# Kernel optimization log

Measured on AMD Instinct MI355X. Metric: run time of the kernel, lower is better.

## Reference

```python
import jax, jax.numpy as jnp
import numpy as np

NEG = -1e10  # the original uses -10000000000.0
B, T, L = 64, 512, 64
START, END = 0, L - 1


def setup_inputs() -> dict:
    key = jax.random.key(0)
    k_em, k_tr, k_len = jax.random.split(key, 3)
    emission_scores = jax.random.normal(k_em, (B, T, L), dtype=jnp.float32)
    # transition initialized as in __init__: randn with start column / end row masked
    transition = jax.random.normal(k_tr, (L, L), dtype=jnp.float32)
    transition = transition.at[:, START].set(NEG)
    transition = transition.at[END, :].set(NEG)
    sent_lens = jax.random.randint(k_len, (B,), T // 2, T + 1, dtype=jnp.int32)
    return {"emission_scores": emission_scores, "transition": transition,
            "sent_lens": sent_lens}


def reference(emission_scores, transition, sent_lens):
    # --- calculate_all_scores ---
    em = emission_scores.at[:, :, START].set(NEG).at[:, :, END].set(NEG)
    # scores[b,t,y_prev,y_t] = transition[y_prev,y_t] + emission[b,t,y_t]
    scores = transition[None, None, :, :] + em[:, :, None, :]  # [B,T,L,L]
    scores = scores.at[:, 1:, START, :].set(NEG)

    # --- forward_score: sequential DP via scan ---
    alpha0 = scores[:, 0, START, :]  # [B,L]

    def step(alpha_prev, s_t):  # s_t: [B,L,L]
        alpha_t = jax.nn.logsumexp(alpha_prev[:, :, None] + s_t, axis=1)
        return alpha_t, alpha_t

    _, alphas_rest = jax.lax.scan(step, alpha0, jnp.moveaxis(scores[:, 1:], 1, 0))
    alpha = jnp.concatenate([alpha0[:, None, :], jnp.moveaxis(alphas_rest, 0, 1)],
                            axis=1)  # [B,T,L]

    idx = (sent_lens - 1).astype(jnp.int32)[:, None, None]  # [B,1,1]
    last_alpha = jnp.take_along_axis(alpha, idx, axis=1)[:, 0, :]  # [B,L]
    last_alpha = last_alpha + transition[:, END][None, :]
    log_Z = jax.nn.logsumexp(last_alpha, axis=1)  # [B]
    return alpha, log_Z
```

## Files before the change

### kernel.cpp

```cpp
#include <hip/hip_runtime.h>

#define NEGV -10000000000.0f
constexpr int Bn = 64, Tn = 512, Ln = 64;
constexpr int CK = 32;
constexpr int NC = 16;
constexpr int QP = 68;

typedef float f32x16 __attribute__((ext_vector_type(16)));
typedef __bf16 bf16x8 __attribute__((ext_vector_type(8)));
typedef unsigned int u32;
typedef unsigned short u16;

__device__ inline float waveMaxF(float v) {
#pragma unroll
    for (int off = 32; off > 0; off >>= 1)
        v = fmaxf(v, __shfl_xor(v, off, 64));
    return v;
}
__device__ inline u32 packbf(float a, float b) {
    u32 ua = __float_as_uint(a) + 0x8000u;
    u32 ub = __float_as_uint(b) + 0x8000u;
    return (ua >> 16) | (ub & 0xffff0000u);
}
__device__ inline float lo16f(u32 d) { return __uint_as_float(d << 16); }
__device__ inline float hi16f(u32 d) { return __uint_as_float(d & 0xffff0000u); }

template <bool FIRST>
__device__ void chunk_scan(const float* __restrict__ emb,
                           float* __restrict__ outb, float* uLDS,
                           const float* Ecol, float entry, int t0, int j, int len,
                           float trSj, float* aLastOut, float* aFinalOut) {
    const bool edge = (j == 0) || (j == Ln - 1);
    float emq[4];
#pragma unroll
    for (int tt = 0; tt < 4; ++tt) {
        float v = emb[(t0 + tt) * Ln + j];
        emq[tt] = edge ? NEGV : v;
    }
    float aPrev, mPrev, u;
    int tauStart;
    if (FIRST) {
        float a0 = trSj + emq[0];
        outb[t0 * Ln + j] = a0;
        aPrev = a0;
        mPrev = __shfl(a0, 1, 64);
        u = __expf(a0 - mPrev);
        tauStart = 1;
    } else {
        aPrev = entry;
        mPrev = __shfl(entry, 1, 64);
        u = __expf(entry - mPrev);
        tauStart = 0;
    }
    float aLast = *aLastOut;
#pragma unroll 4
    for (int tau = tauStart; tau < CK; ++tau) {
        const int t = t0 + tau;
        uLDS[j] = u;
        const float em_t = emq[tau & 3];
        const int tp = tau + 4;
        if (tp < CK) {
            float v = emb[(t0 + tp) * Ln + j];
            emq[tp & 3] = edge ? NEGV : v;
        }
        float mNext = __shfl(aPrev, 1, 64);
        float cf = __expf(em_t + (mPrev - mNext));
        float acc0 = 0.f, acc1 = 0.f, acc2 = 0.f, acc3 = 0.f;
        const float4* u4 = reinterpret_cast<const float4*>(uLDS);
#pragma unroll
        for (int i4 = 0; i4 < 16; ++i4) {
            float4 uv = u4[i4];
            acc0 = fmaf(uv.x, Ecol[4 * i4 + 0], acc0);
            acc1 = fmaf(uv.y, Ecol[4 * i4 + 1], acc1);
            acc2 = fmaf(uv.z, Ecol[4 * i4 + 2], acc2);
            acc3 = fmaf(uv.w, Ecol[4 * i4 + 3], acc3);
        }
        float S = (acc0 + acc1) + (acc2 + acc3);
        float lg = __logf(S);
        lg = (S > 0.f) ? lg : NEGV;
        float a_t = em_t + (mPrev + lg);
        outb[t * Ln + j] = a_t;
        if (t == len - 1) aLast = a_t;
        u = S * cf;
        aPrev = a_t;
        mPrev = mNext;
    }
    *aLastOut = aLast;
    *aFinalOut = aPrev;
}

__global__ __launch_bounds__(128) void crf_passA(const float* __restrict__ em,
                                                 const float* __restrict__ tr,
                                                 float* __restrict__ out,
                                                 float* __restrict__ wsE,
                                                 float* __restrict__ wsS) {
    const int b = blockIdx.x & 63;
    const int cix = blockIdx.x >> 6;
    const int J = threadIdx.x >> 6;
    const int L = threadIdx.x & 63;
    __shared__ alignas(16) float gtab[CK * 64];
    __shared__ alignas(16) u16 Qlds[64 * QP];
    __shared__ alignas(16) float uLDS[64];
    __shared__ float sLDS[2];
    __shared__ float sigLDS[2];

    if (cix == 0) {
        if (J == 1) return;
        float Ecol[Ln];
#pragma unroll
        for (int i = 0; i < Ln; ++i) Ecol[i] = __expf(tr[i * Ln + L]);
        const float trSj = tr[L];
        const float* emb = em + (size_t)b * Tn * Ln;
        float* outb = out + (size_t)b * Tn * Ln;
        float dummyLast = 0.f, aFinal;
        chunk_scan<true>(emb, outb, uLDS, Ecol, 0.f, 0, L,  -1, trSj, &dummyLast, &aFinal);
        wsE[b * 1024 + 1 * 64 + L] = aFinal;
        return;
    }

    const int t0 = CK * cix;
    const int c31 = L & 31;
    const int h = L >> 5;

    {
        float orig[16], sv[16];
        const int tb = t0 + 16 * J;
#pragma unroll
        for (int r = 0; r < 16; ++r) {
            float v = em[((size_t)b * Tn + (tb + r)) * Ln + L];
            if (L == 0 || L == Ln - 1) v = NEGV;
            orig[r] = v;
            sv[r] = v;
        }
#pragma unroll
        for (int off = 32; off > 0; off >>= 1) {
#pragma unroll
            for (int r = 0; r < 16; ++r)
                sv[r] = fmaxf(sv[r], __shfl_xor(sv[r], off, 64));
        }
        float ssum = 0.f;
#pragma unroll
        for (int r = 0; r < 16; ++r) {
            gtab[(16 * J + r) * 64 + L] = __expf(orig[r] - sv[r]);
            ssum += sv[r];
        }
        if (L == 0) sLDS[J] = ssum;
    }
    __syncthreads();
    const float sSum = sLDS[0] + sLDS[1];

    uint4 Ap[2][4];
#pragma unroll
    for (int I = 0; I < 2; ++I)
#pragma unroll
        for (int kc = 0; kc < 4; ++kc) {
            float e[8];
#pragma unroll
            for (int q = 0; q < 8; ++q) {
                int k = 16 * kc + 8 * h + q;
                e[q] = __expf(tr[k * Ln + 32 * I + c31]);
            }
            Ap[I][kc] = make_uint4(packbf(e[0], e[1]), packbf(e[2], e[3]),
                                   packbf(e[4], e[5]), packbf(e[6], e[7]));
        }

    const int n = 32 * J + c31;
    {
        const float* trn = tr + n * Ln + 32 * h;
        const float* g0 = gtab + 32 * h;
#pragma unroll
        for (int k4 = 0; k4 < 8; ++k4) {
            float v0 = __expf(trn[4 * k4 + 0]) * g0[4 * k4 + 0];
            float v1 = __expf(trn[4 * k4 + 1]) * g0[4 * k4 + 1];
            float v2 = __expf(trn[4 * k4 + 2]) * g0[4 * k4 + 2];
            float v3 = __expf(trn[4 * k4 + 3]) * g0[4 * k4 + 3];
            uint2 w;
            w.x = packbf(v0, v1);
            w.y = packbf(v2, v3);
            *(uint2*)&Qlds[n * QP + 32 * h + 4 * k4] = w;
        }
    }

    float sig_w = 0.f;
    float wm = 1.0f;
    const f32x16 Z = (f32x16)(0.0f);
    for (int tau = 1; tau < CK; ++tau) {
        uint4 Bp[4];
#pragma unroll
        for (int kc = 0; kc < 4; ++kc) {
            const u16* p = &Qlds[n * QP + 16 * kc + 8 * h];
            uint2 q0 = *(const uint2*)(p);
            uint2 q1 = *(const uint2*)(p + 4);
            Bp[kc] = make_uint4(q0.x, q0.y, q1.x, q1.y);
        }
        f32x16 acc0 = Z, acc1 = Z;
#pragma unroll
        for (int kc = 0; kc < 4; ++kc) {
            acc0 = __builtin_amdgcn_mfma_f32_32x32x16_bf16(
                __builtin_bit_cast(bf16x8, Ap[0][kc]),
                __builtin_bit_cast(bf16x8, Bp[kc]), acc0, 0, 0, 0);
            acc1 = __builtin_amdgcn_mfma_f32_32x32x16_bf16(
                __builtin_bit_cast(bf16x8, Ap[1][kc]),
                __builtin_bit_cast(bf16x8, Bp[kc]), acc1, 0, 0, 0);
        }
        const bool doRescale = ((tau & 3) == 0);
        const bool doMeasure = ((tau & 3) == 2);
        float rr = 1.0f;
        if (doRescale) {
            rr = 1.0f / wm;
            sig_w += __logf(wm);
        }
        float lmax = 0.f;
#pragma unroll
        for (int I = 0; I < 2; ++I) {
#pragma unroll
            for (int rg = 0; rg < 4; ++rg) {
                const int k0 = 32 * I + 8 * rg + 4 * h;
                float4 G = *(const float4*)&gtab[tau * 64 + k0];
                float v0 = (I ? acc1 : acc0)[4 * rg + 0] * (G.x * rr);
                float v1 = (I ? acc1 : acc0)[4 * rg + 1] * (G.y * rr);
                float v2 = (I ? acc1 : acc0)[4 * rg + 2] * (G.z * rr);
                float v3 = (I ? acc1 : acc0)[4 * rg + 3] * (G.w * rr);
                if (doMeasure) lmax = fmaxf(lmax, fmaxf(fmaxf(v0, v1), fmaxf(v2, v3)));
                uint2 w;
                w.x = packbf(v0, v1);
                w.y = packbf(v2, v3);
                *(uint2*)&Qlds[n * QP + k0] = w;
            }
        }
        if (doMeasure) wm = waveMaxF(lmax);
    }

    if (L == 0) sigLDS[J] = sSum + sig_w;
    __syncthreads();
    const float sg0 = sigLDS[0], sg1 = sigLDS[1];
    const float smax = fmaxf(sg0, sg1);
    const float fh = __expf((h ? sg1 : sg0) - smax);
    const int r = 32 * J + c31;
    float rv[32];
    float lmaxr = 0.f;
#pragma unroll
    for (int i = 0; i < 32; ++i) {
        float v = __uint_as_float(((u32)Qlds[(32 * h + i) * QP + r]) << 16) * fh;
        rv[i] = v;
        lmaxr = fmaxf(lmaxr, v);
    }
    float rmax = fmaxf(lmaxr, __shfl_xor(lmaxr, 32, 64));
    float inv = (rmax > 0.f) ? 1.0f / rmax : 0.f;
    float sj = (rmax > 0.f) ? smax + __logf(rmax) : 0.f;
    u32* og = (u32*)out + (size_t)b * (Tn * Ln) + (size_t)cix * (CK * Ln) + r * 32 + h * 16;
#pragma unroll
    for (int w8 = 0; w8 < 4; ++w8) {
        uint4 w;
        w.x = packbf(rv[8 * w8 + 0] * inv, rv[8 * w8 + 1] * inv);
        w.y = packbf(rv[8 * w8 + 2] * inv, rv[8 * w8 + 3] * inv);
        w.z = packbf(rv[8 * w8 + 4] * inv, rv[8 * w8 + 5] * inv);
        w.w = packbf(rv[8 * w8 + 6] * inv, rv[8 * w8 + 7] * inv);
        *(uint4*)(og + 4 * w8) = w;
    }
    if (h == 0) wsS[b * 1024 + cix * 64 + r] = sj;
}

__global__ __launch_bounds__(64) void crf_passB(const float* __restrict__ out,
                                                float* __restrict__ wsE,
                                                const float* __restrict__ wsS) {
    const int b = blockIdx.x;
    const int j = threadIdx.x;
    __shared__ alignas(16) float uL[64];
    const u32* Qbase = (const u32*)out + (size_t)b * (Tn * Ln);

    float e = wsE[b * 1024 + 1 * 64 + j];
    uint4 nxt[8];
    float signxt = wsS[b * 1024 + 1 * 64 + j];
#pragma unroll
    for (int r = 0; r < 8; ++r) nxt[r] = *(const uint4*)(Qbase + 1 * (CK * Ln) + j * 32 + 4 * r);

#pragma unroll
    for (int c = 1; c <= 14; ++c) {
        uint4 cur[8];
#pragma unroll
        for (int r = 0; r < 8; ++r) cur[r] = nxt[r];
        float sig = signxt;
        if (c < 14) {
#pragma unroll
            for (int r = 0; r < 8; ++r)
                nxt[r] = *(const uint4*)(Qbase + (size_t)(c + 1) * (CK * Ln) + j * 32 + 4 * r);
            signxt = wsS[b * 1024 + (c + 1) * 64 + j];
        }
        float m = __shfl(e, 1, 64);
        uL[j] = __expf(e - m);
        const float4* u4 = reinterpret_cast<const float4*>(uL);
        float S = 0.f;
#pragma unroll
        for (int i4 = 0; i4 < 16; ++i4) {
            float4 uv = u4[i4];
            u32 d0 = ((const u32*)cur)[2 * i4];
            u32 d1 = ((const u32*)cur)[2 * i4 + 1];
            S = fmaf(uv.x, lo16f(d0), S);
            S = fmaf(uv.y, hi16f(d0), S);
            S = fmaf(uv.z, lo16f(d1), S);
            S = fmaf(uv.w, hi16f(d1), S);
        }
        float a;
        if (S > 0.f) a = m + sig + __logf(S);
        else a = m + NEGV + ((j == 0) ? NEGV : 0.f);
        e = a;
        wsE[b * 1024 + (c + 1) * 64 + j] = e;
    }
}

__global__ __launch_bounds__(64) void crf_passC(const float* __restrict__ em,
                                                const float* __restrict__ tr,
                                                const int* __restrict__ lens,
                                                float* __restrict__ out,
                                                const float* __restrict__ wsE) {
    const int b = blockIdx.x & 63;
    const int cix = 1 + (blockIdx.x >> 6);
    const int j = threadIdx.x;
    __shared__ alignas(16) float uLDS[64];

    float Ecol[Ln];
#pragma unroll
    for (int i = 0; i < Ln; ++i) Ecol[i] = __expf(tr[i * Ln + j]);
    const float trEj = tr[j * Ln + (Ln - 1)];
    const int len = lens[b];
    const float* emb = em + (size_t)b * Tn * Ln;
    float* outb = out + (size_t)b * Tn * Ln;
    const float entry = wsE[b * 1024 + cix * 64 + j];

    float aLast = 0.f, aFinal;
    chunk_scan<false>(emb, outb, uLDS, Ecol, entry, CK * cix, j, len, 0.f, &aLast, &aFinal);

    if (((len - 1) >> 5) == cix) {
        float last = aLast + trEj;
        float m2 = last;
#pragma unroll
        for (int off = 32; off > 0; off >>= 1)
            m2 = fmaxf(m2, __shfl_xor(m2, off, 64));
        float e2 = __expf(last - m2);
#pragma unroll
        for (int off = 32; off > 0; off >>= 1)
            e2 += __shfl_xor(e2, off, 64);
        if (j == 0) out[(size_t)Bn * Tn * Ln + b] = m2 + __logf(e2);
    }
}

__global__ __launch_bounds__(64) void crf_fallback(const float* __restrict__ em,
                                                   const float* __restrict__ tr,
                                                   const int* __restrict__ lens,
                                                   float* __restrict__ out) {
    const int b = blockIdx.x;
    const int j = threadIdx.x;
    __shared__ alignas(16) float uLDS[Ln];
    float E[Ln];
#pragma unroll
    for (int i = 0; i < Ln; ++i) E[i] = __expf(tr[i * Ln + j]);
    const float trSj = tr[j];
    const float trEj = tr[j * Ln + (Ln - 1)];
    const int len = lens[b];
    const bool edge = (j == 0) || (j == Ln - 1);
    const float* emb = em + (size_t)b * Tn * Ln;
    float* outb = out + (size_t)b * Tn * Ln;
    float emq[4];
#pragma unroll
    for (int tt = 0; tt < 4; ++tt) {
        float v = emb[tt * Ln + j];
        emq[tt] = edge ? NEGV : v;
    }
    float a = trSj + emq[0];
    outb[j] = a;
    float aPrev = a, aLast = a;
    float mPrev = __shfl(a, 1, 64);
    float u = __expf(a - mPrev);
#pragma unroll 4
    for (int t = 1; t < Tn; ++t) {
        uLDS[j] = u;
        const float em_t = emq[t & 3];
        const int tp = t + 4;
        if (tp < Tn) {
            float v = emb[tp * Ln + j];
            emq[tp & 3] = edge ? NEGV : v;
        }
        float mNext = __shfl(aPrev, 1, 64);
        float cf = __expf(em_t + (mPrev - mNext));
        float acc0 = 0.f, acc1 = 0.f, acc2 = 0.f, acc3 = 0.f;
        const float4* u4 = reinterpret_cast<const float4*>(uLDS);
#pragma unroll
        for (int i4 = 0; i4 < 16; ++i4) {
            float4 uv = u4[i4];
            acc0 = fmaf(uv.x, E[4 * i4 + 0], acc0);
            acc1 = fmaf(uv.y, E[4 * i4 + 1], acc1);
            acc2 = fmaf(uv.z, E[4 * i4 + 2], acc2);
            acc3 = fmaf(uv.w, E[4 * i4 + 3], acc3);
        }
        float S = (acc0 + acc1) + (acc2 + acc3);
        float lg = __logf(S);
        lg = (S > 0.f) ? lg : NEGV;
        float a_t = em_t + (mPrev + lg);
        outb[t * Ln + j] = a_t;
        if (t == len - 1) aLast = a_t;
        u = S * cf;
        aPrev = a_t;
        mPrev = mNext;
    }
    float last = aLast + trEj;
    float m2 = last;
#pragma unroll
    for (int off = 32; off > 0; off >>= 1)
        m2 = fmaxf(m2, __shfl_xor(m2, off, 64));
    float e2 = __expf(last - m2);
#pragma unroll
    for (int off = 32; off > 0; off >>= 1)
        e2 += __shfl_xor(e2, off, 64);
    if (j == 0) out[(size_t)Bn * Tn * Ln + b] = m2 + __logf(e2);
}

extern "C" void kernel_launch(void* const* d_in, const int* in_sizes, int n_in,
                              void* d_out, int out_size, void* d_ws, size_t ws_size,
                              hipStream_t stream) {
    const float* em = (const float*)d_in[0];
    const float* tr = (const float*)d_in[1];
    const int* lens = (const int*)d_in[2];
    float* out = (float*)d_out;
    const size_t wsNeed = 2u * 64 * 16 * 64 * sizeof(float);
    if (ws_size >= wsNeed) {
        float* wsE = (float*)d_ws;
        float* wsS = wsE + 64 * 16 * 64;
        crf_passA<<<dim3(1024), dim3(128), 0, stream>>>(em, tr, out, wsE, wsS);
        crf_passB<<<dim3(64), dim3(64), 0, stream>>>(out, wsE, wsS);
        crf_passC<<<dim3(960), dim3(64), 0, stream>>>(em, tr, lens, out, wsE);
    } else {
        crf_fallback<<<dim3(Bn), dim3(64), 0, stream>>>(em, tr, lens, out);
    }
}
```

Before: 136.5 us.

## Keep MFMA B operand in registers via permlane32 swap instead of LDS round-trip

The per-step write of the bf16 state to LDS followed by reading it back as the next MFMA B operand is replaced. The accumulator output is packed with the hardware v_cvt_pk_bf16_f32 instruction and rearranged across lane halves with permlane32_swap, so it lands directly in the B-operand layout. LDS is written only once after the loop, and the padding QP drops to 64 since the per-step access pattern no longer needs conflict avoidance. Rounding now uses the hardware conversion instead of the manual add-and-shift, and correctness depends on the swap producing exactly the operand layout.

```diff
diff --git a/kernel.cpp b/kernel.cpp
--- a/kernel.cpp
+++ b/kernel.cpp
@@ -4,12 +4,13 @@
 constexpr int Bn = 64, Tn = 512, Ln = 64;
 constexpr int CK = 32;
 constexpr int NC = 16;
-constexpr int QP = 68;
+constexpr int QP = 64;
 
 typedef float f32x16 __attribute__((ext_vector_type(16)));
 typedef __bf16 bf16x8 __attribute__((ext_vector_type(8)));
 typedef unsigned int u32;
 typedef unsigned short u16;
+typedef unsigned int u32x2 __attribute__((ext_vector_type(2)));
 
 __device__ inline float waveMaxF(float v) {
 #pragma unroll
@@ -21,6 +22,16 @@
     u32 ua = __float_as_uint(a) + 0x8000u;
     u32 ub = __float_as_uint(b) + 0x8000u;
     return (ua >> 16) | (ub & 0xffff0000u);
+}
+__device__ inline u32 cvtpk(float a, float b) {
+    u32 r;
+    asm("v_cvt_pk_bf16_f32 %0, %1, %2" : "=v"(r) : "v"(a), "v"(b));
+    return r;
+}
+__device__ inline void swap32(u32& x, u32& y) {
+    u32x2 r = __builtin_amdgcn_permlane32_swap(x, y, false, false);
+    x = r.x;
+    y = r.y;
 }
 __device__ inline float lo16f(u32 d) { return __uint_as_float(d << 16); }
 __device__ inline float hi16f(u32 d) { return __uint_as_float(d & 0xffff0000u); }
@@ -165,19 +176,19 @@
         }
 
     const int n = 32 * J + c31;
+    uint4 Bp[4];
     {
-        const float* trn = tr + n * Ln + 32 * h;
-        const float* g0 = gtab + 32 * h;
-#pragma unroll
-        for (int k4 = 0; k4 < 8; ++k4) {
-            float v0 = __expf(trn[4 * k4 + 0]) * g0[4 * k4 + 0];
-            float v1 = __expf(trn[4 * k4 + 1]) * g0[4 * k4 + 1];
-            float v2 = __expf(trn[4 * k4 + 2]) * g0[4 * k4 + 2];
-            float v3 = __expf(trn[4 * k4 + 3]) * g0[4 * k4 + 3];
-            uint2 w;
-            w.x = packbf(v0, v1);
-            w.y = packbf(v2, v3);
-            *(uint2*)&Qlds[n * QP + 32 * h + 4 * k4] = w;
+        const float* trn = tr + n * Ln;
+#pragma unroll
+        for (int kc = 0; kc < 4; ++kc) {
+            float v[8];
+#pragma unroll
+            for (int q = 0; q < 8; ++q) {
+                const int k = 16 * kc + 8 * h + q;
+                v[q] = __expf(trn[k]) * gtab[k];
+            }
+            Bp[kc] = make_uint4(cvtpk(v[0], v[1]), cvtpk(v[2], v[3]),
+                                cvtpk(v[4], v[5]), cvtpk(v[6], v[7]));
         }
     }
 
@@ -185,14 +196,6 @@
     float wm = 1.0f;
     const f32x16 Z = (f32x16)(0.0f);
     for (int tau = 1; tau < CK; ++tau) {
-        uint4 Bp[4];
-#pragma unroll
-        for (int kc = 0; kc < 4; ++kc) {
-            const u16* p = &Qlds[n * QP + 16 * kc + 8 * h];
-            uint2 q0 = *(const uint2*)(p);
-            uint2 q1 = *(const uint2*)(p + 4);
-            Bp[kc] = make_uint4(q0.x, q0.y, q1.x, q1.y);
-        }
         f32x16 acc0 = Z, acc1 = Z;
 #pragma unroll
         for (int kc = 0; kc < 4; ++kc) {
@@ -211,25 +214,35 @@
             sig_w += __logf(wm);
         }
         float lmax = 0.f;
+        const float* gt = gtab + tau * 64;
 #pragma unroll
         for (int I = 0; I < 2; ++I) {
+            u32 pp[8];
 #pragma unroll
             for (int rg = 0; rg < 4; ++rg) {
                 const int k0 = 32 * I + 8 * rg + 4 * h;
-                float4 G = *(const float4*)&gtab[tau * 64 + k0];
+                float4 G = *(const float4*)&gt[k0];
                 float v0 = (I ? acc1 : acc0)[4 * rg + 0] * (G.x * rr);
                 float v1 = (I ? acc1 : acc0)[4 * rg + 1] * (G.y * rr);
                 float v2 = (I ? acc1 : acc0)[4 * rg + 2] * (G.z * rr);
                 float v3 = (I ? acc1 : acc0)[4 * rg + 3] * (G.w * rr);
                 if (doMeasure) lmax = fmaxf(lmax, fmaxf(fmaxf(v0, v1), fmaxf(v2, v3)));
-                uint2 w;
-                w.x = packbf(v0, v1);
-                w.y = packbf(v2, v3);
-                *(uint2*)&Qlds[n * QP + k0] = w;
+                pp[2 * rg + 0] = cvtpk(v0, v1);
+                pp[2 * rg + 1] = cvtpk(v2, v3);
             }
+            swap32(pp[0], pp[2]);
+            swap32(pp[1], pp[3]);
+            swap32(pp[4], pp[6]);
+            swap32(pp[5], pp[7]);
+            Bp[2 * I + 0] = make_uint4(pp[0], pp[1], pp[2], pp[3]);
+            Bp[2 * I + 1] = make_uint4(pp[4], pp[5], pp[6], pp[7]);
         }
         if (doMeasure) wm = waveMaxF(lmax);
     }
+
+#pragma unroll
+    for (int kc = 0; kc < 4; ++kc)
+        *(uint4*)&Qlds[n * QP + 16 * kc + 8 * h] = Bp[kc];
 
     if (L == 0) sigLDS[J] = sSum + sig_w;
     __syncthreads();
```

Measured after the change: 126.4 us. 1.08x faster.
